# Kernel tuning notes

Measured on AMD Instinct MI355X. Metric: run time of the kernel, lower is better.

The kernel has to match this reference:

```python
import jax, jax.numpy as jnp
from jax import lax
import numpy as np

REG = 0.1        # entropic regularization
ITERS = 50       # Sinkhorn iterations
DS = 8           # avg-pool downsample factor
EPS = 1e-8


def _avg_pool_scaled(x, d):
    # F.avg_pool2d(x, d) * d**2 == sum over non-overlapping dxd windows
    B, C, H, W = x.shape
    return x.reshape(B, C, H // d, d, W // d, d).mean(axis=(3, 5)) * (d * d)


def _cost_matrix(H, W):
    y = jnp.arange(H, dtype=jnp.float32)
    x = jnp.arange(W, dtype=jnp.float32)
    yy, xx = jnp.meshgrid(y, x, indexing='ij')
    coords = jnp.stack([yy.ravel(), xx.ravel()], axis=1)      # [N, 2]
    diff = coords[:, None, :] - coords[None, :, :]            # [N, N, 2]
    return (diff ** 2).sum(axis=-1)                           # [N, N] squared euclidean


def setup_inputs() -> dict:
    key = jax.random.key(0)
    k1, k2 = jax.random.split(key)
    B, H, W = 16, 512, 512
    pred_density = jax.random.uniform(k1, (B, 1, H, W), dtype=jnp.float32)
    gt_density = jax.random.uniform(k2, (B, 1, H, W), dtype=jnp.float32)
    return {"pred_density": pred_density, "gt_density": gt_density}


def reference(pred_density, gt_density):
    pred = _avg_pool_scaled(pred_density, DS)
    gt = _avg_pool_scaled(gt_density, DS)
    B, _, H, W = pred.shape
    N = H * W

    C = _cost_matrix(H, W)          # [N, N]
    K = jnp.exp(-C / REG)           # Gibbs kernel
    M = K * C                       # so cost = u @ (M @ v) == sum(P * C) without materializing P

    a = pred.reshape(B, N)
    b = gt.reshape(B, N)
    a_sum = jnp.clip(a.sum(axis=1), 1e-8, None)
    b_sum = jnp.clip(b.sum(axis=1), 1e-8, None)
    a_n = a / a_sum[:, None]
    b_n = b / b_sum[:, None]

    def sinkhorn_cost(a1, b1):
        def step(carry, _):
            u, v = carry
            v = b1 / (K.T @ u + EPS)
            u = a1 / (K @ v + EPS)
            return (u, v), None
        (u, v), _ = lax.scan(step, (jnp.ones_like(a1), jnp.zeros_like(b1)),
                             None, length=ITERS)
        # P = u[:,None] * K * v[None,:]; (P*C).sum() = u^T (K*C) v
        return u @ (M @ v)

    costs = jax.vmap(sinkhorn_cost)(a_n, b_n)                 # [B]
    valid = (a_sum > 0.5) & (b_sum > 0.5)
    return jnp.where(valid, costs, 0.0).sum() / B
```

## Files before the change

### kernel.cpp

```cpp
#include <hip/hip_runtime.h>


#define G1 4.5399929762484854e-05f
#define EPSF 1e-8f

__device__ __forceinline__ float dpp_shr1(float x) {
  return __int_as_float(__builtin_amdgcn_update_dpp(0, __float_as_int(x), 0x138, 0xF, 0xF, true));
}
__device__ __forceinline__ float dpp_shl1(float x) {
  return __int_as_float(__builtin_amdgcn_update_dpp(0, __float_as_int(x), 0x130, 0xF, 0xF, true));
}

extern "C" __global__ void __launch_bounds__(256)
ot_pool(const float* __restrict__ pred, const float* __restrict__ gt,
        float* __restrict__ ws_pool, double* __restrict__ ws_part) {
  const int bx    = blockIdx.x;
  const int batch = bx & 15;
  const int which = (bx >> 4) & 1;
  const int slice = bx >> 5;
  const float* src  = (which ? gt : pred) + batch * (512 * 512);
  float*       outp = ws_pool + which * (16 * 4096) + batch * 4096;

  double part = 0.0;
  for (int k = 0; k < 2; ++k) {
    const int wi = slice * 512 + k * 256 + threadIdx.x;
    const int y = wi >> 6, x = wi & 63;
    const float* base = src + (y * 8) * 512 + x * 8;
    float s = 0.f;
#pragma unroll
    for (int dy = 0; dy < 8; ++dy) {
      const float4* r4 = (const float4*)(base + dy * 512);
      float4 p0 = r4[0], p1 = r4[1];
      s += ((p0.x + p0.y) + (p0.z + p0.w)) + ((p1.x + p1.y) + (p1.z + p1.w));
    }
    outp[wi] = s;
    part += (double)s;
  }
#pragma unroll
  for (int off = 32; off > 0; off >>= 1) part += __shfl_down(part, off, 64);
  __shared__ double pr[4];
  if ((threadIdx.x & 63) == 0) pr[threadIdx.x >> 6] = part;
  __syncthreads();
  if (threadIdx.x == 0)
    ws_part[slice * 32 + which * 16 + batch] = (pr[0] + pr[1]) + (pr[2] + pr[3]);
}

__device__ __forceinline__ void ot_step(const float (&src)[16], float (&dst)[16],
                                        const float (&wt)[16],
                                        float (*rd)[6][64], float (*wr)[6][64],
                                        int wv, int lane) {
  const float up = rd[1][wv][lane];
  const float dn = rd[0][wv + 2][lane];
#pragma unroll
  for (int r = 1; r < 15; ++r) {
    const float s = (dpp_shr1(src[r]) + dpp_shl1(src[r])) + (src[r - 1] + src[r + 1]);
    dst[r] = wt[r] * __builtin_amdgcn_rcpf(__builtin_fmaf(G1, s, src[r]) + EPSF);
  }
  const float s0 = (dpp_shr1(src[0]) + dpp_shl1(src[0])) + (up + src[1]);
  dst[0] = wt[0] * __builtin_amdgcn_rcpf(__builtin_fmaf(G1, s0, src[0]) + EPSF);
  const float s15 = (dpp_shr1(src[15]) + dpp_shl1(src[15])) + (src[14] + dn);
  dst[15] = wt[15] * __builtin_amdgcn_rcpf(__builtin_fmaf(G1, s15, src[15]) + EPSF);
  wr[0][wv + 1][lane] = dst[0];
  wr[1][wv + 1][lane] = dst[15];
  __syncthreads();
}

extern "C" __global__ void __launch_bounds__(256)
ot_sinkhorn(const float* __restrict__ ws_pool, const double* __restrict__ ws_part,
            float* __restrict__ out) {
  const int batch = blockIdx.x;
  const int lane  = threadIdx.x & 63;
  const int wv    = threadIdx.x >> 6;

  __shared__ float  bnd[2][2][6][64];
  __shared__ double ssh[2];
  __shared__ float  red[4];

  double s = 0.0;
  if (threadIdx.x < 16)
    s = ws_part[(threadIdx.x & 7) * 32 + ((threadIdx.x & 8) ? 16 : 0) + batch];
  s += __shfl_down(s, 4, 64);
  s += __shfl_down(s, 2, 64);
  s += __shfl_down(s, 1, 64);
  if (threadIdx.x == 0) ssh[0] = s;
  if (threadIdx.x == 8) ssh[1] = s;

  bnd[0][0][wv + 1][lane] = 1.0f;
  bnd[0][1][wv + 1][lane] = 1.0f;
  if (wv == 0) {
    bnd[0][1][0][lane] = 0.f; bnd[0][0][5][lane] = 0.f;
    bnd[1][1][0][lane] = 0.f; bnd[1][0][5][lane] = 0.f;
  }
  __syncthreads();

  const float a_sum = (float)ssh[0];
  const float b_sum = (float)ssh[1];
  const float inva = 1.0f / fmaxf(a_sum, 1e-8f);
  const float invb = 1.0f / fmaxf(b_sum, 1e-8f);

  float av[16], bv[16], u[16], v[16];
  const float* pa = ws_pool + batch * 4096;
  const float* pb = ws_pool + 16 * 4096 + batch * 4096;
#pragma unroll
  for (int r = 0; r < 16; ++r) {
    const int idx = (wv * 16 + r) * 64 + lane;
    av[r] = pa[idx] * inva;
    bv[r] = pb[idx] * invb;
    u[r]  = 1.0f;
  }

#pragma unroll 1
  for (int it = 0; it < 50; ++it) {
    ot_step(u, v, bv, bnd[0], bnd[1], wv, lane);
    ot_step(v, u, av, bnd[1], bnd[0], wv, lane);
  }

  const float up = bnd[1][1][wv][lane];
  const float dn = bnd[1][0][wv + 2][lane];
  float acc = 0.f;
#pragma unroll
  for (int r = 0; r < 16; ++r) {
    const float vm = (r == 0)  ? up : v[r - 1];
    const float vp = (r == 15) ? dn : v[r + 1];
    const float sN = (dpp_shr1(v[r]) + dpp_shl1(v[r])) + (vm + vp);
    acc = __builtin_fmaf(u[r], sN, acc);
  }
#pragma unroll
  for (int off = 32; off > 0; off >>= 1) acc += __shfl_down(acc, off, 64);
  if (lane == 0) red[wv] = acc;
  __syncthreads();
  if (threadIdx.x == 0) {
    const float c = G1 * ((red[0] + red[1]) + (red[2] + red[3]));
    const bool valid = (a_sum > 0.5f) && (b_sum > 0.5f);
    if (valid) atomicAdd(out, c * (1.0f / 16.0f));
  }
}

extern "C" void kernel_launch(void* const* d_in, const int* in_sizes, int n_in,
                              void* d_out, int out_size, void* d_ws, size_t ws_size,
                              hipStream_t stream) {
  (void)in_sizes; (void)n_in; (void)out_size; (void)ws_size;
  const float* pred = (const float*)d_in[0];
  const float* gt   = (const float*)d_in[1];

  float*  ws_pool = (float*)d_ws;
  double* ws_part = (double*)((char*)d_ws + 2 * 16 * 4096 * 4);

  hipLaunchKernelGGL(ot_pool,     dim3(256), dim3(256), 0, stream, pred, gt, ws_pool, ws_part);
  hipLaunchKernelGGL(ot_sinkhorn, dim3(16),  dim3(256), 0, stream, ws_pool, ws_part, (float*)d_out);
}
```

Measured before the change: 110.2 us.

## Widen Sinkhorn blocks to 16 waves and double pooling grid

The Sinkhorn kernel now runs each batch with 1024 threads (16 wavefronts), each holding 4 rows instead of 16, which cuts the serial per-iteration work per thread. Boundary exchange through shared memory grows to 18 slots. The pooling kernel launches 512 blocks with one output per thread, and the partial sums are re-indexed to match. The trade-off is that 16 waves must now meet at every barrier, and there are 100 barriers per run.

New measurement: 108.4 us. Within noise of the previous version (-1.7%).

```diff
diff --git a/kernel.cpp b/kernel.cpp
--- a/kernel.cpp
+++ b/kernel.cpp
@@ -14,83 +14,83 @@
 extern "C" __global__ void __launch_bounds__(256)
 ot_pool(const float* __restrict__ pred, const float* __restrict__ gt,
         float* __restrict__ ws_pool, double* __restrict__ ws_part) {
-  const int bx    = blockIdx.x;
-  const int batch = bx & 15;
-  const int which = (bx >> 4) & 1;
-  const int slice = bx >> 5;
-  const float* src  = (which ? gt : pred) + batch * (512 * 512);
-  float*       outp = ws_pool + which * (16 * 4096) + batch * 4096;
+  const int bw    = blockIdx.x >> 4;
+  const int which = bw >> 4;
+  const int batch = bw & 15;
+  const int wi    = ((blockIdx.x & 15) << 8) | threadIdx.x;
+  const float* src = (which ? gt : pred) + batch * (512 * 512);
 
-  double part = 0.0;
-  for (int k = 0; k < 2; ++k) {
-    const int wi = slice * 512 + k * 256 + threadIdx.x;
-    const int y = wi >> 6, x = wi & 63;
-    const float* base = src + (y * 8) * 512 + x * 8;
-    float s = 0.f;
+  const int y = wi >> 6, x = wi & 63;
+  const float* base = src + (y * 8) * 512 + x * 8;
+  float s = 0.f;
 #pragma unroll
-    for (int dy = 0; dy < 8; ++dy) {
-      const float4* r4 = (const float4*)(base + dy * 512);
-      float4 p0 = r4[0], p1 = r4[1];
-      s += ((p0.x + p0.y) + (p0.z + p0.w)) + ((p1.x + p1.y) + (p1.z + p1.w));
-    }
-    outp[wi] = s;
-    part += (double)s;
+  for (int dy = 0; dy < 8; ++dy) {
+    const float4* r4 = (const float4*)(base + dy * 512);
+    float4 p0 = r4[0], p1 = r4[1];
+    s += ((p0.x + p0.y) + (p0.z + p0.w)) + ((p1.x + p1.y) + (p1.z + p1.w));
   }
+  ws_pool[bw * 4096 + wi] = s;
+
+  double part = (double)s;
 #pragma unroll
   for (int off = 32; off > 0; off >>= 1) part += __shfl_down(part, off, 64);
   __shared__ double pr[4];
   if ((threadIdx.x & 63) == 0) pr[threadIdx.x >> 6] = part;
   __syncthreads();
   if (threadIdx.x == 0)
-    ws_part[slice * 32 + which * 16 + batch] = (pr[0] + pr[1]) + (pr[2] + pr[3]);
+    ws_part[blockIdx.x] = (pr[0] + pr[1]) + (pr[2] + pr[3]);
 }
 
-__device__ __forceinline__ void ot_step(const float (&src)[16], float (&dst)[16],
-                                        const float (&wt)[16],
-                                        float (*rd)[6][64], float (*wr)[6][64],
+__device__ __forceinline__ void ot_step(const float (&src)[4], float (&dst)[4],
+                                        const float (&wt)[4],
+                                        float (*rd)[18][64], float (*wr)[18][64],
                                         int wv, int lane) {
   const float up = rd[1][wv][lane];
   const float dn = rd[0][wv + 2][lane];
 #pragma unroll
-  for (int r = 1; r < 15; ++r) {
+  for (int r = 1; r < 3; ++r) {
     const float s = (dpp_shr1(src[r]) + dpp_shl1(src[r])) + (src[r - 1] + src[r + 1]);
     dst[r] = wt[r] * __builtin_amdgcn_rcpf(__builtin_fmaf(G1, s, src[r]) + EPSF);
   }
   const float s0 = (dpp_shr1(src[0]) + dpp_shl1(src[0])) + (up + src[1]);
   dst[0] = wt[0] * __builtin_amdgcn_rcpf(__builtin_fmaf(G1, s0, src[0]) + EPSF);
-  const float s15 = (dpp_shr1(src[15]) + dpp_shl1(src[15])) + (src[14] + dn);
-  dst[15] = wt[15] * __builtin_amdgcn_rcpf(__builtin_fmaf(G1, s15, src[15]) + EPSF);
+  const float s3 = (dpp_shr1(src[3]) + dpp_shl1(src[3])) + (src[2] + dn);
+  dst[3] = wt[3] * __builtin_amdgcn_rcpf(__builtin_fmaf(G1, s3, src[3]) + EPSF);
   wr[0][wv + 1][lane] = dst[0];
-  wr[1][wv + 1][lane] = dst[15];
+  wr[1][wv + 1][lane] = dst[3];
   __syncthreads();
 }
 
-extern "C" __global__ void __launch_bounds__(256)
+extern "C" __global__ void __launch_bounds__(1024)
 ot_sinkhorn(const float* __restrict__ ws_pool, const double* __restrict__ ws_part,
             float* __restrict__ out) {
   const int batch = blockIdx.x;
   const int lane  = threadIdx.x & 63;
   const int wv    = threadIdx.x >> 6;
 
-  __shared__ float  bnd[2][2][6][64];
+  __shared__ float  bnd[2][2][18][64];
   __shared__ double ssh[2];
-  __shared__ float  red[4];
+  __shared__ float  red[16];
 
   double s = 0.0;
-  if (threadIdx.x < 16)
-    s = ws_part[(threadIdx.x & 7) * 32 + ((threadIdx.x & 8) ? 16 : 0) + batch];
-  s += __shfl_down(s, 4, 64);
-  s += __shfl_down(s, 2, 64);
-  s += __shfl_down(s, 1, 64);
-  if (threadIdx.x == 0) ssh[0] = s;
-  if (threadIdx.x == 8) ssh[1] = s;
+  if (threadIdx.x < 32) {
+    const int whichsel = threadIdx.x >> 4;
+    const int sub      = threadIdx.x & 15;
+    s = ws_part[((whichsel * 16 + batch) << 4) | sub];
+  }
+  s += __shfl_down(s, 8, 16);
+  s += __shfl_down(s, 4, 16);
+  s += __shfl_down(s, 2, 16);
+  s += __shfl_down(s, 1, 16);
+  if (threadIdx.x == 0)  ssh[0] = s;
+  if (threadIdx.x == 16) ssh[1] = s;
 
+  if (wv == 0) {
+    bnd[0][1][0][lane] = 0.f; bnd[0][0][17][lane] = 0.f;
+    bnd[1][1][0][lane] = 0.f; bnd[1][0][17][lane] = 0.f;
+  }
   bnd[0][0][wv + 1][lane] = 1.0f;
   bnd[0][1][wv + 1][lane] = 1.0f;
-  if (wv == 0) {
-    bnd[0][1][0][lane] = 0.f; bnd[0][0][5][lane] = 0.f;
-    bnd[1][1][0][lane] = 0.f; bnd[1][0][5][lane] = 0.f;
-  }
   __syncthreads();
 
   const float a_sum = (float)ssh[0];
@@ -98,12 +98,12 @@
   const float inva = 1.0f / fmaxf(a_sum, 1e-8f);
   const float invb = 1.0f / fmaxf(b_sum, 1e-8f);
 
-  float av[16], bv[16], u[16], v[16];
+  float av[4], bv[4], u[4], v[4];
   const float* pa = ws_pool + batch * 4096;
   const float* pb = ws_pool + 16 * 4096 + batch * 4096;
 #pragma unroll
-  for (int r = 0; r < 16; ++r) {
-    const int idx = (wv * 16 + r) * 64 + lane;
+  for (int r = 0; r < 4; ++r) {
+    const int idx = (wv * 4 + r) * 64 + lane;
     av[r] = pa[idx] * inva;
     bv[r] = pb[idx] * invb;
     u[r]  = 1.0f;
@@ -119,9 +119,9 @@
   const float dn = bnd[1][0][wv + 2][lane];
   float acc = 0.f;
 #pragma unroll
-  for (int r = 0; r < 16; ++r) {
-    const float vm = (r == 0)  ? up : v[r - 1];
-    const float vp = (r == 15) ? dn : v[r + 1];
+  for (int r = 0; r < 4; ++r) {
+    const float vm = (r == 0) ? up : v[r - 1];
+    const float vp = (r == 3) ? dn : v[r + 1];
     const float sN = (dpp_shr1(v[r]) + dpp_shl1(v[r])) + (vm + vp);
     acc = __builtin_fmaf(u[r], sN, acc);
   }
@@ -130,7 +130,10 @@
   if (lane == 0) red[wv] = acc;
   __syncthreads();
   if (threadIdx.x == 0) {
-    const float c = G1 * ((red[0] + red[1]) + (red[2] + red[3]));
+    float c = 0.f;
+#pragma unroll
+    for (int w = 0; w < 16; ++w) c += red[w];
+    c *= G1;
     const bool valid = (a_sum > 0.5f) && (b_sum > 0.5f);
     if (valid) atomicAdd(out, c * (1.0f / 16.0f));
   }
@@ -146,6 +149,6 @@
   float*  ws_pool = (float*)d_ws;
   double* ws_part = (double*)((char*)d_ws + 2 * 16 * 4096 * 4);
 
-  hipLaunchKernelGGL(ot_pool,     dim3(256), dim3(256), 0, stream, pred, gt, ws_pool, ws_part);
-  hipLaunchKernelGGL(ot_sinkhorn, dim3(16),  dim3(256), 0, stream, ws_pool, ws_part, (float*)d_out);
+  hipLaunchKernelGGL(ot_pool,     dim3(512), dim3(256),  0, stream, pred, gt, ws_pool, ws_part);
+  hipLaunchKernelGGL(ot_sinkhorn, dim3(16),  dim3(1024), 0, stream, ws_pool, ws_part, (float*)d_out);
 }
```
